# Kernel optimization log

Hardware: AMD Instinct MI355X
Metric: run time of the kernel (lower is better)

Reference implementation:

```python
import jax, jax.numpy as jnp
import numpy as np

NBINS = 256
RGB_W = jnp.array([0.2989, 0.5870, 0.1140], dtype=jnp.float32)  # tf.image.rgb_to_grayscale weights


def _otsu_threshold(g):
    # g: [H, W] grayscale image. skimage-style Otsu: 256 bins over [min, max].
    mn = g.min()
    mx = g.max()
    rng = jnp.maximum(mx - mn, 1e-12)
    idx = jnp.clip(((g - mn) * (NBINS / rng)).astype(jnp.int32), 0, NBINS - 1)
    hist = jnp.zeros((NBINS,), jnp.float32).at[idx.ravel()].add(1.0)
    centers = mn + (jnp.arange(NBINS, dtype=jnp.float32) + 0.5) * (rng / NBINS)
    # class-1: bins [0..t], class-2: bins (t..255]
    w1 = jnp.cumsum(hist)                              # [256]
    w2 = jnp.cumsum(hist[::-1])[::-1]                  # [256]
    hc = hist * centers
    m1 = jnp.cumsum(hc) / jnp.maximum(w1, 1e-12)
    m2 = (jnp.cumsum(hc[::-1]) / jnpveps(w2))[::-1] if False else (jnp.cumsum(hc[::-1]) / jnp.maximum(jnp.cumsum(hist[::-1]), 1e-12))[::-1]
    var12 = w1[:-1] * w2[1:] * (m1[:-1] - m2[1:]) ** 2  # between-class variance, [255]
    return centers[jnp.argmax(var12)]


def setup_inputs() -> dict:
    key = jax.random.key(0)
    x = jax.random.uniform(key, (64, 512, 512, 3), dtype=jnp.float32) * 255.0
    return {"x": x}


def reference(x):
    # grayscale: [B, H, W]
    gray = jnp.einsum("bhwc,c->bhw", x, RGB_W)
    thr = jax.vmap(_otsu_threshold)(gray)              # [B]
    binary = jnp.where(gray > thr[:, None, None], 255.0, 0.0)  # [B, H, W]
    # grayscale_to_rgb: tile channel
    return jnp.broadcast_to(binary[..., None], binary.shape + (3,))
```

## Files before the change

kernel.cpp:

```cpp
#include <hip/hip_runtime.h>
#include <stdint.h>

#define NBINS 256
#define HW    (512 * 512)
#define NIMG  64
#define MMB   64
#define HB    32
#define RB 0
#define GB 1032
#define BB 2064
#define STW 3096
#define FINV 0.00390625

__device__ __forceinline__ double gray_of(float r, float g, float b) {
    return fma((double)b, (double)0.1140f,
           fma((double)g, (double)0.5870f,
               (double)r * (double)0.2989f));
}

__device__ __forceinline__ void stage3(const float4* __restrict__ xv, int64_t tile4,
                                       float* __restrict__ st, int tid) {
    #pragma unroll
    for (int k = 0; k < 3; ++k) {
        const int q = k * 256 + tid;
        const float4 v = xv[tile4 + q];
        const int f0 = q * 4;
        int p = (int)(((unsigned)f0 * 21846u) >> 16);
        int c = f0 - 3 * p;
        const float e[4] = {v.x, v.y, v.z, v.w};
        #pragma unroll
        for (int j = 0; j < 4; ++j) {
            const int base = (c == 0) ? RB : ((c == 1) ? GB : BB);
            st[base + p] = e[j];
            if (++c == 3) { c = 0; ++p; }
        }
    }
}

template <bool WF>
__global__ __launch_bounds__(256) void k_minmax(const float* __restrict__ x,
                                                double* __restrict__ mm_part,
                                                unsigned long long* __restrict__ fid4) {
    __shared__ float st[STW];
    __shared__ double smn[4], smx[4];
    const int tid = threadIdx.x;
    const int img = blockIdx.x >> 6;
    const int blk = blockIdx.x & 63;
    const int64_t img4 = (int64_t)img * (HW * 3 / 4);
    const float4* xv = (const float4*)x;
    double mn = 1e300, mx = -1e300;
    for (int it = 0; it < 4; ++it) {
        const int tl = blk * 4 + it;
        stage3(xv, img4 + (int64_t)tl * 768, st, tid);
        __syncthreads();
        const float4 R = *(const float4*)&st[RB + 4 * tid];
        const float4 G = *(const float4*)&st[GB + 4 * tid];
        const float4 B = *(const float4*)&st[BB + 4 * tid];
        const double g0 = gray_of(R.x, G.x, B.x), g1 = gray_of(R.y, G.y, B.y),
                     g2 = gray_of(R.z, G.z, B.z), g3 = gray_of(R.w, G.w, B.w);
        mn = fmin(mn, fmin(fmin(g0, g1), fmin(g2, g3)));
        mx = fmax(mx, fmax(fmax(g0, g1), fmax(g2, g3)));
        if (WF) {
            const unsigned long long f0 = (unsigned long long)(unsigned)(g0 * 256.0);
            const unsigned long long f1 = (unsigned long long)(unsigned)(g1 * 256.0);
            const unsigned long long f2 = (unsigned long long)(unsigned)(g2 * 256.0);
            const unsigned long long f3 = (unsigned long long)(unsigned)(g3 * 256.0);
            fid4[img * (HW / 4) + tl * 256 + tid] = f0 | (f1 << 16) | (f2 << 32) | (f3 << 48);
        }
        __syncthreads();
    }
    #pragma unroll
    for (int off = 32; off; off >>= 1) {
        mn = fmin(mn, __shfl_xor(mn, off));
        mx = fmax(mx, __shfl_xor(mx, off));
    }
    if ((tid & 63) == 0) { smn[tid >> 6] = mn; smx[tid >> 6] = mx; }
    __syncthreads();
    if (tid == 0) {
        mn = fmin(fmin(smn[0], smn[1]), fmin(smn[2], smn[3]));
        mx = fmax(fmax(smx[0], smx[1]), fmax(smx[2], smx[3]));
        mm_part[(img * MMB + blk) * 2 + 0] = mn;
        mm_part[(img * MMB + blk) * 2 + 1] = mx;
    }
}

__device__ __forceinline__ void mm_reduce(const double* __restrict__ mm_part, int img,
                                          int tid, double* __restrict__ sdm) {
    if (tid < 64) {
        double mn = mm_part[(img * MMB + tid) * 2 + 0];
        double mx = mm_part[(img * MMB + tid) * 2 + 1];
        #pragma unroll
        for (int off = 32; off; off >>= 1) {
            mn = fmin(mn, __shfl_xor(mn, off));
            mx = fmax(mx, __shfl_xor(mx, off));
        }
        if (tid == 0) { sdm[0] = mn; sdm[1] = mx; }
    }
}

__device__ __forceinline__ int bin_of(double g, double mn, double s) {
    int id = (int)__dmul_rn(__dsub_rn(g, mn), s);
    return id < 0 ? 0 : (id > 255 ? 255 : id);
}

template <bool UF>
__global__ __launch_bounds__(256) void k_hist(const unsigned long long* __restrict__ fid4,
        const float* __restrict__ x, const double* __restrict__ mm_part,
        unsigned* __restrict__ hist_part) {
    __shared__ float st[STW];
    __shared__ unsigned lh[NBINS];
    __shared__ double sdm[2];
    const int tid = threadIdx.x;
    const int img = blockIdx.x >> 5;
    const int blk = blockIdx.x & 31;
    lh[tid] = 0u;
    mm_reduce(mm_part, img, tid, sdm);
    __syncthreads();
    const double mn = sdm[0];
    const double s  = 256.0 / fmax(__dsub_rn(sdm[1], mn), 1e-12);
    const int64_t img4 = (int64_t)img * (HW * 3 / 4);
    const float4* xv = (const float4*)x;
    for (int it = 0; it < 8; ++it) {
        const int tl = blk * 8 + it;
        if (UF) {
            const unsigned long long pk = fid4[img * (HW / 4) + tl * 256 + tid];
            #pragma unroll
            for (int j = 0; j < 4; ++j) {
                const unsigned f = (unsigned)(pk >> (16 * j)) & 0xFFFFu;
                const double glo = (double)f * FINV;
                const double ghi = (double)(f + 1) * FINV;
                const int clo = bin_of(glo, mn, s);
                const int chi = bin_of(ghi, mn, s);
                int id;
                if (clo == chi) id = clo;
                else {
                    const int64_t p = (int64_t)img * HW + (int64_t)tl * 1024 + 4 * tid + j;
                    id = bin_of(gray_of(x[3 * p], x[3 * p + 1], x[3 * p + 2]), mn, s);
                }
                atomicAdd(&lh[id], 1u);
            }
        } else {
            stage3(xv, img4 + (int64_t)tl * 768, st, tid);
            __syncthreads();
            const float4 R = *(const float4*)&st[RB + 4 * tid];
            const float4 G = *(const float4*)&st[GB + 4 * tid];
            const float4 B = *(const float4*)&st[BB + 4 * tid];
            atomicAdd(&lh[bin_of(gray_of(R.x, G.x, B.x), mn, s)], 1u);
            atomicAdd(&lh[bin_of(gray_of(R.y, G.y, B.y), mn, s)], 1u);
            atomicAdd(&lh[bin_of(gray_of(R.z, G.z, B.z), mn, s)], 1u);
            atomicAdd(&lh[bin_of(gray_of(R.w, G.w, B.w), mn, s)], 1u);
            __syncthreads();
        }
    }
    __syncthreads();
    hist_part[(img * HB + blk) * NBINS + tid] = lh[tid];
}

__global__ void k_otsu(const unsigned* __restrict__ hist_part,
                       const double* __restrict__ mm_part,
                       double* __restrict__ thr) {
    __shared__ double h[NBINS], w2s[NBINS], m2s[NBINS], vv[NBINS];
    __shared__ double sdm[2];
    const int img = blockIdx.x, t = threadIdx.x;
    mm_reduce(mm_part, img, t, sdm);
    unsigned hu = 0;
    for (int b = 0; b < HB; ++b) hu += hist_part[(img * HB + b) * NBINS + t];
    h[t] = (double)hu;
    __syncthreads();
    const double mn   = sdm[0];
    const double rng  = fmax(__dsub_rn(sdm[1], mn), 1e-12);
    const double step = rng / 256.0;
    double w1 = 0.0, hc1 = 0.0;
    for (int j = 0; j <= t; ++j) {
        const double c = __dadd_rn(mn, __dmul_rn((double)j + 0.5, step));
        w1  = __dadd_rn(w1, h[j]);
        hc1 = __dadd_rn(hc1, __dmul_rn(h[j], c));
    }
    const double m1 = hc1 / fmax(w1, 1e-12);
    double w2 = 0.0, hc2 = 0.0;
    for (int j = NBINS - 1; j >= t; --j) {
        const double c = __dadd_rn(mn, __dmul_rn((double)j + 0.5, step));
        w2  = __dadd_rn(w2, h[j]);
        hc2 = __dadd_rn(hc2, __dmul_rn(h[j], c));
    }
    w2s[t] = w2;
    m2s[t] = hc2 / fmax(w2, 1e-12);
    __syncthreads();
    if (t < NBINS - 1) {
        const double d = __dsub_rn(m1, m2s[t + 1]);
        vv[t] = __dmul_rn(__dmul_rn(w1, w2s[t + 1]), __dmul_rn(d, d));
    }
    __syncthreads();
    if (t == 0) {
        double best = -1.0; int bi = 0;
        for (int i = 0; i < NBINS - 1; ++i)
            if (vv[i] > best) { best = vv[i]; bi = i; }
        thr[img] = __dadd_rn(mn, __dmul_rn((double)bi + 0.5, step));
    }
}

template <bool UF>
__global__ __launch_bounds__(256) void k_binarize(const unsigned long long* __restrict__ fid4,
        const float* __restrict__ x, const double* __restrict__ thr,
        float* __restrict__ out) {
    __shared__ float st[STW];
    __shared__ float bst[1024];
    const int tid = threadIdx.x;
    const int img = blockIdx.x >> 6;
    const int blk = blockIdx.x & 63;
    const double T = thr[img];
    const int64_t img4 = (int64_t)img * (HW * 3 / 4);
    const float4* xv = (const float4*)x;
    float4* ov = (float4*)out;
    for (int it = 0; it < 4; ++it) {
        const int tl = blk * 4 + it;
        float bb[4];
        if (UF) {
            const unsigned long long pk = fid4[img * (HW / 4) + tl * 256 + tid];
            #pragma unroll
            for (int j = 0; j < 4; ++j) {
                const unsigned f = (unsigned)(pk >> (16 * j)) & 0xFFFFu;
                const double glo = (double)f * FINV;
                const double ghi = (double)(f + 1) * FINV;
                float r;
                if (glo > T)       r = 255.f;
                else if (ghi <= T) r = 0.f;
                else {
                    const int64_t p = (int64_t)img * HW + (int64_t)tl * 1024 + 4 * tid + j;
                    const double g = gray_of(x[3 * p], x[3 * p + 1], x[3 * p + 2]);
                    r = (g > T) ? 255.f : 0.f;
                }
                bb[j] = r;
            }
        } else {
            stage3(xv, img4 + (int64_t)tl * 768, st, tid);
            __syncthreads();
            const float4 R = *(const float4*)&st[RB + 4 * tid];
            const float4 G = *(const float4*)&st[GB + 4 * tid];
            const float4 B = *(const float4*)&st[BB + 4 * tid];
            bb[0] = (gray_of(R.x, G.x, B.x) > T) ? 255.f : 0.f;
            bb[1] = (gray_of(R.y, G.y, B.y) > T) ? 255.f : 0.f;
            bb[2] = (gray_of(R.z, G.z, B.z) > T) ? 255.f : 0.f;
            bb[3] = (gray_of(R.w, G.w, B.w) > T) ? 255.f : 0.f;
        }
        *(float4*)&bst[4 * tid] = make_float4(bb[0], bb[1], bb[2], bb[3]);
        __syncthreads();
        const int64_t ob4 = img4 + (int64_t)tl * 768;
        #pragma unroll
        for (int k = 0; k < 3; ++k) {
            const int q  = k * 256 + tid;
            const int p0 = (int)(((unsigned)(q * 4) * 21846u) >> 16);
            const int m  = q - 3 * (int)(((unsigned)q * 21846u) >> 16);
            const float lo = bst[p0];
            const float hi = bst[p0 + 1 < 1024 ? p0 + 1 : 1023];
            float4 o;
            o.x = lo;
            o.y = (m + 1 >= 3) ? hi : lo;
            o.z = (m + 2 >= 3) ? hi : lo;
            o.w = (m + 3 >= 3) ? hi : lo;
            ov[ob4 + q] = o;
        }
        __syncthreads();
    }
}

extern "C" void kernel_launch(void* const* d_in, const int* in_sizes, int n_in,
                              void* d_out, int out_size, void* d_ws, size_t ws_size,
                              hipStream_t stream) {
    const float* x = (const float*)d_in[0];
    float* out = (float*)d_out;
    uint8_t* ws = (uint8_t*)d_ws;

    double*             thr       = (double*)(ws);
    double*             mm_part   = (double*)(ws + 1024);
    unsigned*           hist_part = (unsigned*)(ws + 66560);
    unsigned long long* fid4      = (unsigned long long*)(ws + 2163712);
    const bool uf = ws_size >= (size_t)2163712 + (size_t)NIMG * HW * 2;

    if (uf) k_minmax<true ><<<NIMG * MMB, 256, 0, stream>>>(x, mm_part, fid4);
    else    k_minmax<false><<<NIMG * MMB, 256, 0, stream>>>(x, mm_part, nullptr);
    if (uf) k_hist<true ><<<NIMG * HB, 256, 0, stream>>>(fid4, x, mm_part, hist_part);
    else    k_hist<false><<<NIMG * HB, 256, 0, stream>>>(nullptr, x, mm_part, hist_part);
    k_otsu<<<NIMG, 256, 0, stream>>>(hist_part, mm_part, thr);
    if (uf) k_binarize<true ><<<NIMG * MMB, 256, 0, stream>>>(fid4, x, thr, out);
    else    k_binarize<false><<<NIMG * MMB, 256, 0, stream>>>(nullptr, x, thr, out);
}
```

Measured before the change: 137.0 us.

## Fuse Otsu threshold into binarize kernel and stage input via direct LDS loads

Merges the per-image Otsu threshold computation into the binarize kernel, so each of the 64 blocks per image recomputes the threshold from the partial histograms and one launch plus its serialization point go away. Input tiles are now copied linearly into shared memory, using global_load_lds when the builtin exists, instead of being deinterleaved into R/G/B planes. Pixel ownership per thread becomes strided (tid + 256*j), and the non-workspace fallback path is dropped. In exchange the 256-iteration serial prefix loops run redundantly in every binarize block, and linear LDS reads at stride 3 may cause bank conflicts.

```diff
diff --git a/kernel.cpp b/kernel.cpp
--- a/kernel.cpp
+++ b/kernel.cpp
@@ -6,11 +6,17 @@
 #define NIMG  64
 #define MMB   64
 #define HB    32
-#define RB 0
-#define GB 1032
-#define BB 2064
-#define STW 3096
-#define FINV 0.00390625
+#define STW   3072
+#define FINV  0.00390625
+
+#if defined(__has_builtin)
+# if __has_builtin(__builtin_amdgcn_global_load_lds)
+#  define HAVE_GLL 1
+# endif
+#endif
+#ifndef HAVE_GLL
+# define HAVE_GLL 0
+#endif
 
 __device__ __forceinline__ double gray_of(float r, float g, float b) {
     return fma((double)b, (double)0.1140f,
@@ -18,55 +24,49 @@
                (double)r * (double)0.2989f));
 }
 
-__device__ __forceinline__ void stage3(const float4* __restrict__ xv, int64_t tile4,
-                                       float* __restrict__ st, int tid) {
+__device__ __forceinline__ void stage_lin(const float* __restrict__ tp,
+                                          float* __restrict__ st, int tid) {
+#if HAVE_GLL
     #pragma unroll
     for (int k = 0; k < 3; ++k) {
-        const int q = k * 256 + tid;
-        const float4 v = xv[tile4 + q];
-        const int f0 = q * 4;
-        int p = (int)(((unsigned)f0 * 21846u) >> 16);
-        int c = f0 - 3 * p;
-        const float e[4] = {v.x, v.y, v.z, v.w};
-        #pragma unroll
-        for (int j = 0; j < 4; ++j) {
-            const int base = (c == 0) ? RB : ((c == 1) ? GB : BB);
-            st[base + p] = e[j];
-            if (++c == 3) { c = 0; ++p; }
-        }
-    }
-}
-
-template <bool WF>
+        const float* g = tp + (k * 256 + tid) * 4;
+        __builtin_amdgcn_global_load_lds(
+            (__attribute__((address_space(1))) void*)(void*)g,
+            (__attribute__((address_space(3))) void*)(void*)(st + (k * 256 + tid) * 4),
+            16, 0, 0);
+    }
+#else
+    #pragma unroll
+    for (int k = 0; k < 3; ++k) {
+        const float4 v = ((const float4*)tp)[k * 256 + tid];
+        *(float4*)&st[(k * 256 + tid) * 4] = v;
+    }
+#endif
+}
+
 __global__ __launch_bounds__(256) void k_minmax(const float* __restrict__ x,
-                                                double* __restrict__ mm_part,
-                                                unsigned long long* __restrict__ fid4) {
+        double* __restrict__ mm_part, unsigned long long* __restrict__ fid4) {
     __shared__ float st[STW];
     __shared__ double smn[4], smx[4];
     const int tid = threadIdx.x;
     const int img = blockIdx.x >> 6;
     const int blk = blockIdx.x & 63;
-    const int64_t img4 = (int64_t)img * (HW * 3 / 4);
-    const float4* xv = (const float4*)x;
+    const int64_t imgf = (int64_t)img * ((int64_t)HW * 3);
     double mn = 1e300, mx = -1e300;
     for (int it = 0; it < 4; ++it) {
         const int tl = blk * 4 + it;
-        stage3(xv, img4 + (int64_t)tl * 768, st, tid);
-        __syncthreads();
-        const float4 R = *(const float4*)&st[RB + 4 * tid];
-        const float4 G = *(const float4*)&st[GB + 4 * tid];
-        const float4 B = *(const float4*)&st[BB + 4 * tid];
-        const double g0 = gray_of(R.x, G.x, B.x), g1 = gray_of(R.y, G.y, B.y),
-                     g2 = gray_of(R.z, G.z, B.z), g3 = gray_of(R.w, G.w, B.w);
-        mn = fmin(mn, fmin(fmin(g0, g1), fmin(g2, g3)));
-        mx = fmax(mx, fmax(fmax(g0, g1), fmax(g2, g3)));
-        if (WF) {
-            const unsigned long long f0 = (unsigned long long)(unsigned)(g0 * 256.0);
-            const unsigned long long f1 = (unsigned long long)(unsigned)(g1 * 256.0);
-            const unsigned long long f2 = (unsigned long long)(unsigned)(g2 * 256.0);
-            const unsigned long long f3 = (unsigned long long)(unsigned)(g3 * 256.0);
-            fid4[img * (HW / 4) + tl * 256 + tid] = f0 | (f1 << 16) | (f2 << 32) | (f3 << 48);
-        }
+        stage_lin(x + imgf + (int64_t)tl * 3072, st, tid);
+        __syncthreads();
+        unsigned long long pk = 0;
+        #pragma unroll
+        for (int j = 0; j < 4; ++j) {
+            const int w = 3 * tid + 768 * j;
+            const double g = gray_of(st[w], st[w + 1], st[w + 2]);
+            mn = fmin(mn, g);
+            mx = fmax(mx, g);
+            pk |= (unsigned long long)(unsigned)(g * 256.0) << (16 * j);
+        }
+        fid4[img * (HW / 4) + tl * 256 + tid] = pk;
         __syncthreads();
     }
     #pragma unroll
@@ -103,11 +103,9 @@
     return id < 0 ? 0 : (id > 255 ? 255 : id);
 }
 
-template <bool UF>
 __global__ __launch_bounds__(256) void k_hist(const unsigned long long* __restrict__ fid4,
         const float* __restrict__ x, const double* __restrict__ mm_part,
         unsigned* __restrict__ hist_part) {
-    __shared__ float st[STW];
     __shared__ unsigned lh[NBINS];
     __shared__ double sdm[2];
     const int tid = threadIdx.x;
@@ -118,132 +116,94 @@
     __syncthreads();
     const double mn = sdm[0];
     const double s  = 256.0 / fmax(__dsub_rn(sdm[1], mn), 1e-12);
-    const int64_t img4 = (int64_t)img * (HW * 3 / 4);
-    const float4* xv = (const float4*)x;
     for (int it = 0; it < 8; ++it) {
         const int tl = blk * 8 + it;
-        if (UF) {
-            const unsigned long long pk = fid4[img * (HW / 4) + tl * 256 + tid];
-            #pragma unroll
-            for (int j = 0; j < 4; ++j) {
-                const unsigned f = (unsigned)(pk >> (16 * j)) & 0xFFFFu;
-                const double glo = (double)f * FINV;
-                const double ghi = (double)(f + 1) * FINV;
-                const int clo = bin_of(glo, mn, s);
-                const int chi = bin_of(ghi, mn, s);
-                int id;
-                if (clo == chi) id = clo;
-                else {
-                    const int64_t p = (int64_t)img * HW + (int64_t)tl * 1024 + 4 * tid + j;
-                    id = bin_of(gray_of(x[3 * p], x[3 * p + 1], x[3 * p + 2]), mn, s);
-                }
-                atomicAdd(&lh[id], 1u);
+        const unsigned long long pk = fid4[img * (HW / 4) + tl * 256 + tid];
+        #pragma unroll
+        for (int j = 0; j < 4; ++j) {
+            const unsigned f = (unsigned)(pk >> (16 * j)) & 0xFFFFu;
+            const int clo = bin_of((double)f * FINV, mn, s);
+            const int chi = bin_of((double)(f + 1) * FINV, mn, s);
+            int id;
+            if (clo == chi) id = clo;
+            else {
+                const int64_t p = (int64_t)img * HW + (int64_t)tl * 1024 + tid + 256 * j;
+                id = bin_of(gray_of(x[3 * p], x[3 * p + 1], x[3 * p + 2]), mn, s);
             }
-        } else {
-            stage3(xv, img4 + (int64_t)tl * 768, st, tid);
-            __syncthreads();
-            const float4 R = *(const float4*)&st[RB + 4 * tid];
-            const float4 G = *(const float4*)&st[GB + 4 * tid];
-            const float4 B = *(const float4*)&st[BB + 4 * tid];
-            atomicAdd(&lh[bin_of(gray_of(R.x, G.x, B.x), mn, s)], 1u);
-            atomicAdd(&lh[bin_of(gray_of(R.y, G.y, B.y), mn, s)], 1u);
-            atomicAdd(&lh[bin_of(gray_of(R.z, G.z, B.z), mn, s)], 1u);
-            atomicAdd(&lh[bin_of(gray_of(R.w, G.w, B.w), mn, s)], 1u);
-            __syncthreads();
+            atomicAdd(&lh[id], 1u);
         }
     }
     __syncthreads();
     hist_part[(img * HB + blk) * NBINS + tid] = lh[tid];
 }
 
-__global__ void k_otsu(const unsigned* __restrict__ hist_part,
-                       const double* __restrict__ mm_part,
-                       double* __restrict__ thr) {
+__global__ __launch_bounds__(256) void k_bin(const unsigned long long* __restrict__ fid4,
+        const float* __restrict__ x, const double* __restrict__ mm_part,
+        const unsigned* __restrict__ hist_part, float* __restrict__ out) {
     __shared__ double h[NBINS], w2s[NBINS], m2s[NBINS], vv[NBINS];
     __shared__ double sdm[2];
-    const int img = blockIdx.x, t = threadIdx.x;
-    mm_reduce(mm_part, img, t, sdm);
+    __shared__ double sT;
+    __shared__ float bst[1024];
+    const int tid = threadIdx.x;
+    const int img = blockIdx.x >> 6;
+    const int blk = blockIdx.x & 63;
+    mm_reduce(mm_part, img, tid, sdm);
     unsigned hu = 0;
-    for (int b = 0; b < HB; ++b) hu += hist_part[(img * HB + b) * NBINS + t];
-    h[t] = (double)hu;
+    for (int b = 0; b < HB; ++b) hu += hist_part[(img * HB + b) * NBINS + tid];
+    h[tid] = (double)hu;
     __syncthreads();
     const double mn   = sdm[0];
     const double rng  = fmax(__dsub_rn(sdm[1], mn), 1e-12);
     const double step = rng / 256.0;
     double w1 = 0.0, hc1 = 0.0;
-    for (int j = 0; j <= t; ++j) {
+    for (int j = 0; j <= tid; ++j) {
         const double c = __dadd_rn(mn, __dmul_rn((double)j + 0.5, step));
         w1  = __dadd_rn(w1, h[j]);
         hc1 = __dadd_rn(hc1, __dmul_rn(h[j], c));
     }
     const double m1 = hc1 / fmax(w1, 1e-12);
     double w2 = 0.0, hc2 = 0.0;
-    for (int j = NBINS - 1; j >= t; --j) {
+    for (int j = NBINS - 1; j >= tid; --j) {
         const double c = __dadd_rn(mn, __dmul_rn((double)j + 0.5, step));
         w2  = __dadd_rn(w2, h[j]);
         hc2 = __dadd_rn(hc2, __dmul_rn(h[j], c));
     }
-    w2s[t] = w2;
-    m2s[t] = hc2 / fmax(w2, 1e-12);
-    __syncthreads();
-    if (t < NBINS - 1) {
-        const double d = __dsub_rn(m1, m2s[t + 1]);
-        vv[t] = __dmul_rn(__dmul_rn(w1, w2s[t + 1]), __dmul_rn(d, d));
-    }
-    __syncthreads();
-    if (t == 0) {
+    w2s[tid] = w2;
+    m2s[tid] = hc2 / fmax(w2, 1e-12);
+    __syncthreads();
+    if (tid < NBINS - 1) {
+        const double d = __dsub_rn(m1, m2s[tid + 1]);
+        vv[tid] = __dmul_rn(__dmul_rn(w1, w2s[tid + 1]), __dmul_rn(d, d));
+    }
+    __syncthreads();
+    if (tid == 0) {
         double best = -1.0; int bi = 0;
         for (int i = 0; i < NBINS - 1; ++i)
             if (vv[i] > best) { best = vv[i]; bi = i; }
-        thr[img] = __dadd_rn(mn, __dmul_rn((double)bi + 0.5, step));
-    }
-}
-
-template <bool UF>
-__global__ __launch_bounds__(256) void k_binarize(const unsigned long long* __restrict__ fid4,
-        const float* __restrict__ x, const double* __restrict__ thr,
-        float* __restrict__ out) {
-    __shared__ float st[STW];
-    __shared__ float bst[1024];
-    const int tid = threadIdx.x;
-    const int img = blockIdx.x >> 6;
-    const int blk = blockIdx.x & 63;
-    const double T = thr[img];
+        sT = __dadd_rn(mn, __dmul_rn((double)bi + 0.5, step));
+    }
+    __syncthreads();
+    const double T = sT;
     const int64_t img4 = (int64_t)img * (HW * 3 / 4);
-    const float4* xv = (const float4*)x;
     float4* ov = (float4*)out;
     for (int it = 0; it < 4; ++it) {
         const int tl = blk * 4 + it;
-        float bb[4];
-        if (UF) {
-            const unsigned long long pk = fid4[img * (HW / 4) + tl * 256 + tid];
-            #pragma unroll
-            for (int j = 0; j < 4; ++j) {
-                const unsigned f = (unsigned)(pk >> (16 * j)) & 0xFFFFu;
-                const double glo = (double)f * FINV;
-                const double ghi = (double)(f + 1) * FINV;
-                float r;
-                if (glo > T)       r = 255.f;
-                else if (ghi <= T) r = 0.f;
-                else {
-                    const int64_t p = (int64_t)img * HW + (int64_t)tl * 1024 + 4 * tid + j;
-                    const double g = gray_of(x[3 * p], x[3 * p + 1], x[3 * p + 2]);
-                    r = (g > T) ? 255.f : 0.f;
-                }
-                bb[j] = r;
+        const unsigned long long pk = fid4[img * (HW / 4) + tl * 256 + tid];
+        #pragma unroll
+        for (int j = 0; j < 4; ++j) {
+            const unsigned f = (unsigned)(pk >> (16 * j)) & 0xFFFFu;
+            const double glo = (double)f * FINV;
+            const double ghi = (double)(f + 1) * FINV;
+            float r;
+            if (glo > T)       r = 255.f;
+            else if (ghi <= T) r = 0.f;
+            else {
+                const int64_t p = (int64_t)img * HW + (int64_t)tl * 1024 + tid + 256 * j;
+                const double g = gray_of(x[3 * p], x[3 * p + 1], x[3 * p + 2]);
+                r = (g > T) ? 255.f : 0.f;
             }
-        } else {
-            stage3(xv, img4 + (int64_t)tl * 768, st, tid);
-            __syncthreads();
-            const float4 R = *(const float4*)&st[RB + 4 * tid];
-            const float4 G = *(const float4*)&st[GB + 4 * tid];
-            const float4 B = *(const float4*)&st[BB + 4 * tid];
-            bb[0] = (gray_of(R.x, G.x, B.x) > T) ? 255.f : 0.f;
-            bb[1] = (gray_of(R.y, G.y, B.y) > T) ? 255.f : 0.f;
-            bb[2] = (gray_of(R.z, G.z, B.z) > T) ? 255.f : 0.f;
-            bb[3] = (gray_of(R.w, G.w, B.w) > T) ? 255.f : 0.f;
-        }
-        *(float4*)&bst[4 * tid] = make_float4(bb[0], bb[1], bb[2], bb[3]);
+            bst[tid + 256 * j] = r;
+        }
         __syncthreads();
         const int64_t ob4 = img4 + (int64_t)tl * 768;
         #pragma unroll
@@ -271,17 +231,11 @@
     float* out = (float*)d_out;
     uint8_t* ws = (uint8_t*)d_ws;
 
-    double*             thr       = (double*)(ws);
-    double*             mm_part   = (double*)(ws + 1024);
-    unsigned*           hist_part = (unsigned*)(ws + 66560);
-    unsigned long long* fid4      = (unsigned long long*)(ws + 2163712);
-    const bool uf = ws_size >= (size_t)2163712 + (size_t)NIMG * HW * 2;
-
-    if (uf) k_minmax<true ><<<NIMG * MMB, 256, 0, stream>>>(x, mm_part, fid4);
-    else    k_minmax<false><<<NIMG * MMB, 256, 0, stream>>>(x, mm_part, nullptr);
-    if (uf) k_hist<true ><<<NIMG * HB, 256, 0, stream>>>(fid4, x, mm_part, hist_part);
-    else    k_hist<false><<<NIMG * HB, 256, 0, stream>>>(nullptr, x, mm_part, hist_part);
-    k_otsu<<<NIMG, 256, 0, stream>>>(hist_part, mm_part, thr);
-    if (uf) k_binarize<true ><<<NIMG * MMB, 256, 0, stream>>>(fid4, x, thr, out);
-    else    k_binarize<false><<<NIMG * MMB, 256, 0, stream>>>(nullptr, x, thr, out);
-}
+    double*             mm_part   = (double*)(ws);
+    unsigned*           hist_part = (unsigned*)(ws + 65536);
+    unsigned long long* fid4      = (unsigned long long*)(ws + 2162688);
+
+    k_minmax<<<NIMG * MMB, 256, 0, stream>>>(x, mm_part, fid4);
+    k_hist<<<NIMG * HB, 256, 0, stream>>>(fid4, x, mm_part, hist_part);
+    k_bin<<<NIMG * MMB, 256, 0, stream>>>(fid4, x, mm_part, hist_part, out);
+}
```

Measured after the change: 163.1 us. +19.1%, slower.
